# Optimization experiments

Hardware: AMD Instinct MI355X
Metric: run time of the kernel (lower is better)

The kernel has to match this reference:

```python
import jax, jax.numpy as jnp
import numpy as np

B = 8192
DIMS = [1024, 1024, 1024, 1024]  # input, hidden0, hidden1, output
RANK = 64


def _apg_layer(x, Wm, bm, U, V, b, activate):
    # hyper-net (MLP_Layer with no hidden units == single Linear): generates rank*rank weights per sample
    w = (x @ Wm.T + bm).reshape(x.shape[0], RANK, RANK)   # [B, r, r]
    u = x @ U.T                                           # U_matrix: [B, r]
    # (u.unsqueeze(-1) * w).sum(-2) == per-sample matvec
    h = jnp.einsum('br,brs->bs', u, w)                    # [B, r]
    out = h @ V.T + b                                     # V_matrix + static bias: [B, out]
    return jax.nn.relu(out) if activate else out


def setup_inputs() -> dict:
    key = jax.random.key(0)
    ks = jax.random.split(key, 16)
    inp = {"x": jax.random.normal(ks[0], (B, DIMS[0]), dtype=jnp.float32)}
    ki = 1
    for l in range(3):
        din, dout = DIMS[l], DIMS[l + 1]
        inp[f"Wm{l}"] = jax.random.normal(ks[ki], (RANK * RANK, din), dtype=jnp.float32) * (1.0 / np.sqrt(din)); ki += 1
        inp[f"bm{l}"] = jnp.zeros((RANK * RANK,), dtype=jnp.float32)
        inp[f"U{l}"] = jax.random.normal(ks[ki], (RANK, din), dtype=jnp.float32) * (1.0 / np.sqrt(din)); ki += 1
        inp[f"V{l}"] = jax.random.normal(ks[ki], (dout, RANK), dtype=jnp.float32) * (1.0 / np.sqrt(RANK)); ki += 1
        inp[f"b{l}"] = jnp.zeros((dout,), dtype=jnp.float32)
    return inp


def reference(x, Wm0, bm0, U0, V0, b0, Wm1, bm1, U1, V1, b1, Wm2, bm2, U2, V2, b2):
    h = _apg_layer(x, Wm0, bm0, U0, V0, b0, activate=True)   # hidden layer 0 + ReLU
    h = _apg_layer(h, Wm1, bm1, U1, V1, b1, activate=True)   # hidden layer 1 + ReLU
    out = _apg_layer(h, Wm2, bm2, U2, V2, b2, activate=False)  # output layer, no activation
    return out
```

## Files before the change

kernel.cpp:

```cpp
#include <hip/hip_runtime.h>
#include <stdint.h>

typedef short bf16x8_t __attribute__((ext_vector_type(8)));
typedef short bf16x4_t __attribute__((ext_vector_type(4)));
typedef float f32x4_t __attribute__((ext_vector_type(4)));
typedef unsigned short u16x4_t __attribute__((ext_vector_type(4)));

#define DEV static __device__ __forceinline__

DEV float bf2f(unsigned short u) {
  union { unsigned int i; float f; } v; v.i = ((unsigned int)u) << 16; return v.f;
}
DEV unsigned short f2bf(float f) {
  union { float f; unsigned int i; } v; v.f = f;
  unsigned int x = v.i;
  unsigned int lsb = (x >> 16) & 1u;
  x += 0x7fffu + lsb;
  return (unsigned short)(x >> 16);
}

struct CvtTab {
  const float* src[10];
  unsigned short* dst[10];
  int bstart[10];
};

__global__ __launch_bounds__(256) void cvt_all_k(CvtTab t) {
  int bi = blockIdx.x;
  int seg = 0;
#pragma unroll
  for (int s = 1; s < 10; s++) seg += (bi >= t.bstart[s]) ? 1 : 0;
  int local = (bi - t.bstart[seg]) * 256 + threadIdx.x;
  const float* src = t.src[seg];
  unsigned short* dst = t.dst[seg];
  float4 v = ((const float4*)src)[local];
  u16x4_t o = { f2bf(v.x), f2bf(v.y), f2bf(v.z), f2bf(v.w) };
  *(u16x4_t*)&dst[local * 4] = o;
}

__global__ __launch_bounds__(256, 2) void u_splitk(
    const unsigned short* __restrict__ A,
    const unsigned short* __restrict__ Ub,
    float* __restrict__ part) {
  __shared__ unsigned short As[128 * 64];
  __shared__ unsigned short Us[64 * 64];

  const int tid = threadIdx.x;
  const int lane = tid & 63;
  const int w = tid >> 6;
  const int rowBase = blockIdx.y * 128;
  const int kBase = blockIdx.x * 256;

  const int rl = lane >> 3;
  const int kbs = lane & 7;
  const int kbg = kbs ^ rl;
  const int fr = lane & 15;
  const int quad = lane >> 4;

  f32x4_t acc[2][4];
#pragma unroll
  for (int i = 0; i < 2; i++)
#pragma unroll
    for (int j = 0; j < 4; j++) acc[i][j] = f32x4_t{0.f, 0.f, 0.f, 0.f};

  for (int kt = kBase; kt < kBase + 256; kt += 64) {
    __syncthreads();
#pragma unroll
    for (int jj = 0; jj < 4; ++jj) {
      int tr = w * 32 + jj * 8 + rl;
      const unsigned short* ga = A + (size_t)(rowBase + tr) * 1024 + kt + kbg * 8;
      __builtin_amdgcn_global_load_lds(
          (const __attribute__((address_space(1))) void*)ga,
          (__attribute__((address_space(3))) void*)&As[(w * 32 + jj * 8) * 64],
          16, 0, 0);
    }
#pragma unroll
    for (int jj = 0; jj < 2; ++jj) {
      int tr = w * 16 + jj * 8 + rl;
      const unsigned short* gu = Ub + (size_t)tr * 1024 + kt + kbg * 8;
      __builtin_amdgcn_global_load_lds(
          (const __attribute__((address_space(1))) void*)gu,
          (__attribute__((address_space(3))) void*)&Us[(w * 16 + jj * 8) * 64],
          16, 0, 0);
    }
    __syncthreads();

#pragma unroll
    for (int ks = 0; ks < 2; ++ks) {
      bf16x8_t a[2], b[4];
#pragma unroll
      for (int i = 0; i < 2; i++) {
        int m = w * 32 + i * 16 + fr;
        int slot = (ks * 4 + quad) ^ (m & 7);
        a[i] = *(const bf16x8_t*)&As[m * 64 + slot * 8];
      }
#pragma unroll
      for (int j = 0; j < 4; j++) {
        int n = j * 16 + fr;
        int slot = (ks * 4 + quad) ^ (n & 7);
        b[j] = *(const bf16x8_t*)&Us[n * 64 + slot * 8];
      }
#pragma unroll
      for (int i = 0; i < 2; i++)
#pragma unroll
        for (int j = 0; j < 4; j++)
          acc[i][j] = __builtin_amdgcn_mfma_f32_16x16x32_bf16(a[i], b[j],
                                                              acc[i][j], 0, 0, 0);
    }
  }

  float* pp = part + ((size_t)blockIdx.x * 8192 + rowBase) * 64;
#pragma unroll
  for (int i = 0; i < 2; i++)
#pragma unroll
    for (int j = 0; j < 4; j++)
#pragma unroll
      for (int r = 0; r < 4; r++) {
        int row = w * 32 + i * 16 + quad * 4 + r;
        pp[(size_t)row * 64 + j * 16 + fr] = acc[i][j][r];
      }
}

__global__ __launch_bounds__(256) void u_reduce_k(
    const float* __restrict__ part, unsigned short* __restrict__ ug) {
  int i = blockIdx.x * 256 + threadIdx.x;
  float4 s0 = ((const float4*)part)[i];
  float4 s1 = ((const float4*)part)[i + 131072];
  float4 s2 = ((const float4*)part)[i + 262144];
  float4 s3 = ((const float4*)part)[i + 393216];
  u16x4_t o = { f2bf(s0.x + s1.x + s2.x + s3.x),
                f2bf(s0.y + s1.y + s2.y + s3.y),
                f2bf(s0.z + s1.z + s2.z + s3.z),
                f2bf(s0.w + s1.w + s2.w + s3.w) };
  *(u16x4_t*)&ug[i * 4] = o;
}

template <int OUTF32, int RELU, int BIAS>
__global__ __launch_bounds__(256, 2) void gemm_bt(
    const unsigned short* __restrict__ A, const unsigned short* __restrict__ B,
    const float* __restrict__ bias, void* __restrict__ Cout,
    int M, int N, int K) {
  __shared__ unsigned short As[128 * 64];
  __shared__ unsigned short Bs[128 * 64];

  const int tid = threadIdx.x;
  const int lane = tid & 63;
  const int w = tid >> 6;
  const int wrow0 = (w & 1) * 64;
  const int wcol0 = (w >> 1) * 64;
  const int rowBase = blockIdx.y * 128;
  const int colBase = blockIdx.x * 128;

  const int rl = lane >> 3;
  const int kbs = lane & 7;
  const int kbg = kbs ^ rl;
  const int fr = lane & 15;
  const int quad = lane >> 4;

  f32x4_t acc[4][4];
#pragma unroll
  for (int i = 0; i < 4; i++)
#pragma unroll
    for (int j = 0; j < 4; j++) acc[i][j] = f32x4_t{0.f, 0.f, 0.f, 0.f};

  for (int kt = 0; kt < K; kt += 64) {
    __syncthreads();
#pragma unroll
    for (int jj = 0; jj < 4; ++jj) {
      int tr = w * 32 + jj * 8 + rl;
      const unsigned short* ga = A + (size_t)(rowBase + tr) * K + kt + kbg * 8;
      const unsigned short* gb = B + (size_t)(colBase + tr) * K + kt + kbg * 8;
      __builtin_amdgcn_global_load_lds(
          (const __attribute__((address_space(1))) void*)ga,
          (__attribute__((address_space(3))) void*)&As[(w * 32 + jj * 8) * 64],
          16, 0, 0);
      __builtin_amdgcn_global_load_lds(
          (const __attribute__((address_space(1))) void*)gb,
          (__attribute__((address_space(3))) void*)&Bs[(w * 32 + jj * 8) * 64],
          16, 0, 0);
    }
    __syncthreads();

#pragma unroll
    for (int ks = 0; ks < 2; ++ks) {
      bf16x8_t a[4], b[4];
#pragma unroll
      for (int i = 0; i < 4; i++) {
        int m = wrow0 + i * 16 + fr;
        int slot = (ks * 4 + quad) ^ (m & 7);
        a[i] = *(const bf16x8_t*)&As[m * 64 + slot * 8];
      }
#pragma unroll
      for (int j = 0; j < 4; j++) {
        int n = wcol0 + j * 16 + fr;
        int slot = (ks * 4 + quad) ^ (n & 7);
        b[j] = *(const bf16x8_t*)&Bs[n * 64 + slot * 8];
      }
#pragma unroll
      for (int i = 0; i < 4; i++)
#pragma unroll
        for (int j = 0; j < 4; j++)
          acc[i][j] = __builtin_amdgcn_mfma_f32_16x16x32_bf16(a[i], b[j],
                                                              acc[i][j], 0, 0, 0);
    }
  }

#pragma unroll
  for (int j = 0; j < 4; j++) {
    int col = colBase + wcol0 + j * 16 + fr;
    float bv = BIAS ? bias[col] : 0.0f;
#pragma unroll
    for (int i = 0; i < 4; i++) {
#pragma unroll
      for (int r = 0; r < 4; r++) {
        int row = rowBase + wrow0 + i * 16 + quad * 4 + r;
        float v = acc[i][j][r] + bv;
        if (RELU) v = v > 0.f ? v : 0.f;
        if (OUTF32)
          ((float*)Cout)[(size_t)row * N + col] = v;
        else
          ((unsigned short*)Cout)[(size_t)row * N + col] = f2bf(v);
      }
    }
  }
}

__global__ __launch_bounds__(256, 2) void gemm_fused(
    const unsigned short* __restrict__ A,
    const unsigned short* __restrict__ Wmb,
    const unsigned short* __restrict__ ug,
    const float* __restrict__ bm,
    unsigned short* __restrict__ h_out) {
  __shared__ unsigned short smem[16384];
  unsigned short* As = smem;
  unsigned short* Bs = smem + 8192;
  const int K = 1024;

  const int tid = threadIdx.x;
  const int lane = tid & 63;
  const int w = tid >> 6;
  const int wrow0 = (w & 1) * 64;
  const int wcol0 = (w >> 1) * 64;
  const int rowBase = blockIdx.y * 128;
  const int colBase = blockIdx.x * 128;

  const int rl = lane >> 3;
  const int kbs = lane & 7;
  const int kbg = kbs ^ rl;
  const int fr = lane & 15;
  const int quad = lane >> 4;

  f32x4_t acc[4][4];
#pragma unroll
  for (int i = 0; i < 4; i++)
#pragma unroll
    for (int j = 0; j < 4; j++) acc[i][j] = f32x4_t{0.f, 0.f, 0.f, 0.f};

  for (int kt = 0; kt < K; kt += 64) {
    __syncthreads();
#pragma unroll
    for (int jj = 0; jj < 4; ++jj) {
      int tr = w * 32 + jj * 8 + rl;
      int ct = colBase + tr;
      int pr = ((ct & 63) << 6) | (ct >> 6);
      const unsigned short* ga = A + (size_t)(rowBase + tr) * K + kt + kbg * 8;
      const unsigned short* gb = Wmb + (size_t)pr * K + kt + kbg * 8;
      __builtin_amdgcn_global_load_lds(
          (const __attribute__((address_space(1))) void*)ga,
          (__attribute__((address_space(3))) void*)&As[(w * 32 + jj * 8) * 64],
          16, 0, 0);
      __builtin_amdgcn_global_load_lds(
          (const __attribute__((address_space(1))) void*)gb,
          (__attribute__((address_space(3))) void*)&Bs[(w * 32 + jj * 8) * 64],
          16, 0, 0);
    }
    __syncthreads();

#pragma unroll
    for (int ks = 0; ks < 2; ++ks) {
      bf16x8_t a[4], b[4];
#pragma unroll
      for (int i = 0; i < 4; i++) {
        int m = wrow0 + i * 16 + fr;
        int slot = (ks * 4 + quad) ^ (m & 7);
        a[i] = *(const bf16x8_t*)&As[m * 64 + slot * 8];
      }
#pragma unroll
      for (int j = 0; j < 4; j++) {
        int n = wcol0 + j * 16 + fr;
        int slot = (ks * 4 + quad) ^ (n & 7);
        b[j] = *(const bf16x8_t*)&Bs[n * 64 + slot * 8];
      }
#pragma unroll
      for (int i = 0; i < 4; i++)
#pragma unroll
        for (int j = 0; j < 4; j++)
          acc[i][j] = __builtin_amdgcn_mfma_f32_16x16x32_bf16(a[i], b[j],
                                                              acc[i][j], 0, 0, 0);
    }
  }

  __syncthreads();

  {
    int row = tid >> 1;
    int c0 = (tid & 1) * 32;
    const unsigned short* up = ug + (size_t)(rowBase + row) * 64 + c0;
    bf16x8_t v0 = *(const bf16x8_t*)(up);
    bf16x8_t v1 = *(const bf16x8_t*)(up + 8);
    bf16x8_t v2 = *(const bf16x8_t*)(up + 16);
    bf16x8_t v3 = *(const bf16x8_t*)(up + 24);
#pragma unroll
    for (int m = 0; m < 8; m++) {
      smem[(c0 + m) * 136 + row] = (unsigned short)v0[m];
      smem[(c0 + 8 + m) * 136 + row] = (unsigned short)v1[m];
      smem[(c0 + 16 + m) * 136 + row] = (unsigned short)v2[m];
      smem[(c0 + 24 + m) * 136 + row] = (unsigned short)v3[m];
    }
  }
  __syncthreads();

  const int s = blockIdx.x * 2 + (w >> 1);
  float bmv[4];
#pragma unroll
  for (int j = 0; j < 4; j++) bmv[j] = bm[(j * 16 + fr) * 64 + s];

#pragma unroll
  for (int i = 0; i < 4; i++) {
    int row0 = wrow0 + i * 16 + quad * 4;
    bf16x4_t uv[4];
#pragma unroll
    for (int j = 0; j < 4; j++)
      uv[j] = *(const bf16x4_t*)&smem[(j * 16 + fr) * 136 + row0];
#pragma unroll
    for (int r = 0; r < 4; r++) {
      float p = 0.f;
#pragma unroll
      for (int j = 0; j < 4; j++)
        p += bf2f((unsigned short)uv[j][r]) * (acc[i][j][r] + bmv[j]);
      p += __shfl_xor(p, 1, 64);
      p += __shfl_xor(p, 2, 64);
      p += __shfl_xor(p, 4, 64);
      p += __shfl_xor(p, 8, 64);
      if (fr == 0)
        h_out[(size_t)(rowBase + row0 + r) * 64 + s] = f2bf(p);
    }
  }
}

extern "C" void kernel_launch(void* const* d_in, const int* in_sizes, int n_in,
                              void* d_out, int out_size, void* d_ws,
                              size_t ws_size, hipStream_t stream) {
  const float* x = (const float*)d_in[0];
  const float* Wm[3] = {(const float*)d_in[1], (const float*)d_in[6], (const float*)d_in[11]};
  const float* bm[3] = {(const float*)d_in[2], (const float*)d_in[7], (const float*)d_in[12]};
  const float* U[3]  = {(const float*)d_in[3], (const float*)d_in[8], (const float*)d_in[13]};
  const float* V[3]  = {(const float*)d_in[4], (const float*)d_in[9], (const float*)d_in[14]};
  const float* bs[3] = {(const float*)d_in[5], (const float*)d_in[10], (const float*)d_in[15]};

  char* p = (char*)d_ws;
  unsigned short* xb = (unsigned short*)p;  p += 8192UL * 1024 * 2;
  unsigned short* act = (unsigned short*)p; p += 8192UL * 1024 * 2;
  unsigned short* Wmb[3];
  for (int l = 0; l < 3; l++) { Wmb[l] = (unsigned short*)p; p += 4096UL * 1024 * 2; }
  unsigned short* Ub[3];
  for (int l = 0; l < 3; l++) { Ub[l] = (unsigned short*)p; p += 64UL * 1024 * 2; }
  unsigned short* Vb[3];
  for (int l = 0; l < 3; l++) { Vb[l] = (unsigned short*)p; p += 1024UL * 64 * 2; }
  unsigned short* hb = (unsigned short*)p;  p += 8192UL * 64 * 2;
  unsigned short* ug = (unsigned short*)p;  p += 8192UL * 64 * 2;
  float* ug_part = (float*)p;               p += 4UL * 8192 * 64 * 4;

  CvtTab t;
  t.src[0] = x;  t.dst[0] = xb;
  for (int l = 0; l < 3; l++) { t.src[1 + l] = Wm[l]; t.dst[1 + l] = Wmb[l]; }
  for (int l = 0; l < 3; l++) { t.src[4 + l] = U[l];  t.dst[4 + l] = Ub[l]; }
  for (int l = 0; l < 3; l++) { t.src[7 + l] = V[l];  t.dst[7 + l] = Vb[l]; }
  int bs_tab[10] = {8192, 4096, 4096, 4096, 64, 64, 64, 64, 64, 64};
  int acc_b = 0;
  for (int s = 0; s < 10; s++) { t.bstart[s] = acc_b; acc_b += bs_tab[s]; }
  cvt_all_k<<<acc_b, 256, 0, stream>>>(t);

  const unsigned short* cur = xb;
  for (int l = 0; l < 3; l++) {
    u_splitk<<<dim3(4, 64), 256, 0, stream>>>(cur, Ub[l], ug_part);
    u_reduce_k<<<512, 256, 0, stream>>>(ug_part, ug);
    gemm_fused<<<dim3(32, 64), 256, 0, stream>>>(cur, Wmb[l], ug, bm[l], hb);
    if (l < 2) {
      gemm_bt<0, 1, 1><<<dim3(8, 64), 256, 0, stream>>>(
          hb, Vb[l], bs[l], act, 8192, 1024, 64);
      cur = act;
    } else {
      gemm_bt<1, 0, 1><<<dim3(8, 64), 256, 0, stream>>>(
          hb, Vb[2], bs[2], d_out, 8192, 1024, 64);
    }
  }
}
```

Measured before the change: 422.1 us.

## Fuse V projection with next layer's U projection in one kernel

Adds a kernel that computes each 16-row tile of act = relu(h·V^T + b), writes it out, and at the same time multiplies the tile still held in LDS by the next layer's U to produce u for the following layer. This replaces the separate gemm_bt plus split-K u GEMM and reduce launches for layers 1 and 2, so the activation does not have to be re-read from global memory to compute u. The cost is a less tiled V GEMM with only 16 rows per block and repeated reads of V and U from global memory in every block.

After: 420.9 us. About the same (-0.3%).

```diff
diff --git a/kernel.cpp b/kernel.cpp
--- a/kernel.cpp
+++ b/kernel.cpp
@@ -348,6 +348,100 @@
   }
 }
 
+__global__ __launch_bounds__(256, 2) void vu_fused(
+    const unsigned short* __restrict__ h,
+    const unsigned short* __restrict__ Vb,
+    const float* __restrict__ bias,
+    const unsigned short* __restrict__ Un,
+    unsigned short* __restrict__ act,
+    unsigned short* __restrict__ u_out) {
+  __shared__ unsigned short tlds[4 * 16 * 72];
+  __shared__ float upart[4 * 16 * 68];
+
+  const int tid = threadIdx.x;
+  const int lane = tid & 63;
+  const int w = tid >> 6;
+  const int fr = lane & 15;
+  const int quad = lane >> 4;
+  const int rowBase = blockIdx.x * 16;
+
+  unsigned short* tl = &tlds[w * 16 * 72];
+
+  bf16x8_t ah0 = *(const bf16x8_t*)&h[(size_t)(rowBase + fr) * 64 + quad * 8];
+  bf16x8_t ah1 = *(const bf16x8_t*)&h[(size_t)(rowBase + fr) * 64 + 32 + quad * 8];
+
+  f32x4_t uacc[4];
+#pragma unroll
+  for (int n = 0; n < 4; n++) uacc[n] = f32x4_t{0.f, 0.f, 0.f, 0.f};
+
+  for (int it = 0; it < 4; ++it) {
+    const int cb = w * 256 + it * 64;
+
+    f32x4_t tacc[4];
+#pragma unroll
+    for (int nt = 0; nt < 4; nt++) {
+      const unsigned short* vrow = Vb + (size_t)(cb + nt * 16 + fr) * 64;
+      bf16x8_t b0 = *(const bf16x8_t*)&vrow[quad * 8];
+      bf16x8_t b1 = *(const bf16x8_t*)&vrow[32 + quad * 8];
+      f32x4_t z = {0.f, 0.f, 0.f, 0.f};
+      z = __builtin_amdgcn_mfma_f32_16x16x32_bf16(ah0, b0, z, 0, 0, 0);
+      tacc[nt] = __builtin_amdgcn_mfma_f32_16x16x32_bf16(ah1, b1, z, 0, 0, 0);
+    }
+
+#pragma unroll
+    for (int nt = 0; nt < 4; nt++) {
+      float bv = bias[cb + nt * 16 + fr];
+#pragma unroll
+      for (int r = 0; r < 4; r++) {
+        float v = tacc[nt][r] + bv;
+        v = v > 0.f ? v : 0.f;
+        tl[(quad * 4 + r) * 72 + nt * 16 + fr] = f2bf(v);
+      }
+    }
+
+    {
+      int m2 = lane >> 2;
+      int kc = (lane & 3) * 16;
+      bf16x8_t t0 = *(const bf16x8_t*)&tl[m2 * 72 + kc];
+      bf16x8_t t1 = *(const bf16x8_t*)&tl[m2 * 72 + kc + 8];
+      unsigned short* ap = act + (size_t)(rowBase + m2) * 1024 + cb + kc;
+      *(bf16x8_t*)ap = t0;
+      *(bf16x8_t*)(ap + 8) = t1;
+    }
+
+#pragma unroll
+    for (int ks = 0; ks < 2; ++ks) {
+      bf16x8_t at = *(const bf16x8_t*)&tl[fr * 72 + ks * 32 + quad * 8];
+#pragma unroll
+      for (int n = 0; n < 4; n++) {
+        bf16x8_t bu = *(const bf16x8_t*)&Un[(size_t)(n * 16 + fr) * 1024 + cb +
+                                            ks * 32 + quad * 8];
+        uacc[n] = __builtin_amdgcn_mfma_f32_16x16x32_bf16(at, bu, uacc[n], 0, 0, 0);
+      }
+    }
+  }
+
+  {
+    float* up = &upart[w * 16 * 68];
+#pragma unroll
+    for (int n = 0; n < 4; n++)
+#pragma unroll
+      for (int r = 0; r < 4; r++)
+        up[(quad * 4 + r) * 68 + n * 16 + fr] = uacc[n][r];
+  }
+  __syncthreads();
+  {
+    int m = tid >> 4;
+    int c0 = (tid & 15) * 4;
+    f32x4_t s = {0.f, 0.f, 0.f, 0.f};
+#pragma unroll
+    for (int wv = 0; wv < 4; wv++)
+      s += *(const f32x4_t*)&upart[wv * 16 * 68 + m * 68 + c0];
+    u16x4_t o = { f2bf(s[0]), f2bf(s[1]), f2bf(s[2]), f2bf(s[3]) };
+    *(u16x4_t*)&u_out[(size_t)(rowBase + m) * 64 + c0] = o;
+  }
+}
+
 extern "C" void kernel_launch(void* const* d_in, const int* in_sizes, int n_in,
                               void* d_out, int out_size, void* d_ws,
                               size_t ws_size, hipStream_t stream) {
@@ -381,14 +475,14 @@
   for (int s = 0; s < 10; s++) { t.bstart[s] = acc_b; acc_b += bs_tab[s]; }
   cvt_all_k<<<acc_b, 256, 0, stream>>>(t);
 
+  u_splitk<<<dim3(4, 64), 256, 0, stream>>>(xb, Ub[0], ug_part);
+  u_reduce_k<<<512, 256, 0, stream>>>(ug_part, ug);
+
   const unsigned short* cur = xb;
   for (int l = 0; l < 3; l++) {
-    u_splitk<<<dim3(4, 64), 256, 0, stream>>>(cur, Ub[l], ug_part);
-    u_reduce_k<<<512, 256, 0, stream>>>(ug_part, ug);
     gemm_fused<<<dim3(32, 64), 256, 0, stream>>>(cur, Wmb[l], ug, bm[l], hb);
     if (l < 2) {
-      gemm_bt<0, 1, 1><<<dim3(8, 64), 256, 0, stream>>>(
-          hb, Vb[l], bs[l], act, 8192, 1024, 64);
+      vu_fused<<<512, 256, 0, stream>>>(hb, Vb[l], bs[l], Ub[l + 1], act, ug);
       cur = act;
     } else {
       gemm_bt<1, 0, 1><<<dim3(8, 64), 256, 0, stream>>>(
```
